# Optimization experiments

Measured on AMD Instinct MI355X. Metric: run time of the kernel, lower is better.

Reference implementation:

```python
import jax, jax.numpy as jnp
import numpy as np

NUM_BUCKETS = 32
MAX_DISTANCE = 128


def _relative_position_bucket(relative_position):
    # bidirectional=True variant of T5's bucketing
    n = -relative_position
    num_buckets = NUM_BUCKETS // 2
    ret = (n < 0).astype(jnp.int32) * num_buckets
    n = jnp.abs(n)
    max_exact = num_buckets // 2
    is_small = n < max_exact
    # log-spaced buckets for large distances
    val_if_large = max_exact + (
        jnp.log(jnp.maximum(n, 1).astype(jnp.float32) / max_exact)
        / np.log(MAX_DISTANCE / max_exact)
        * (num_buckets - max_exact)
    ).astype(jnp.int32)
    val_if_large = jnp.minimum(val_if_large, num_buckets - 1)
    return ret + jnp.where(is_small, n, val_if_large)


def setup_inputs() -> dict:
    key = jax.random.key(0)
    ks = jax.random.split(key, 6)
    B, S, D, H, DK = 4, 1024, 1024, 16, 64
    inner = H * DK
    s = 1.0 / np.sqrt(D).astype(np.float32)
    x = jax.random.normal(ks[0], (B, S, D), jnp.float32)
    Wq = jax.random.normal(ks[1], (D, inner), jnp.float32) * s
    Wk = jax.random.normal(ks[2], (D, inner), jnp.float32) * s
    Wv = jax.random.normal(ks[3], (D, inner), jnp.float32) * s
    Wo = jax.random.normal(ks[4], (inner, D), jnp.float32) * s
    rel_emb = jax.random.normal(ks[5], (NUM_BUCKETS, H), jnp.float32) * 0.02
    return {"x": x, "Wq": Wq, "Wk": Wk, "Wv": Wv, "Wo": Wo, "rel_emb": rel_emb}


def reference(x, Wq, Wk, Wv, Wo, rel_emb):
    B, S, D = x.shape
    H = rel_emb.shape[1]
    DK = Wq.shape[1] // H

    def shape_heads(t):  # [B,S,H*DK] -> [B,H,S,DK]
        return t.reshape(B, S, H, DK).transpose(0, 2, 1, 3)

    q = shape_heads(x @ Wq)
    k = shape_heads(x @ Wk)
    v = shape_heads(x @ Wv)

    # note: T5 does NOT scale by 1/sqrt(d_kv)
    scores = jnp.einsum("bhqd,bhkd->bhqk", q, k)

    pos = jnp.arange(S)
    rel = pos[None, :] - pos[:, None]            # memory - query
    bucket = _relative_position_bucket(rel)      # [S,S] int32
    bias = rel_emb[bucket].transpose(2, 0, 1)[None]  # [1,H,S,S]

    weights = jax.nn.softmax(scores + bias, axis=-1)
    ctx = jnp.einsum("bhqk,bhkd->bhqd", weights, v)
    ctx = ctx.transpose(0, 2, 1, 3).reshape(B, S, H * DK)
    return ctx @ Wo
```

## Files before the change

### kernel.cpp

```cpp
#include <hip/hip_runtime.h>
#include <math.h>

#define B_ 4
#define S_ 1024
#define D_ 1024
#define H_ 16
#define DK_ 64

typedef short bf16x8 __attribute__((ext_vector_type(8)));
typedef float f32x4 __attribute__((ext_vector_type(4)));

__device__ __forceinline__ unsigned short f2bf(float f) {
    unsigned int u = __float_as_uint(f);
    u = (u + 0x7FFFu + ((u >> 16) & 1u)) >> 16;
    return (unsigned short)u;
}

__device__ __forceinline__ float exp2_fast(float x) {
#if __has_builtin(__builtin_amdgcn_exp2f)
    return __builtin_amdgcn_exp2f(x);
#else
    return exp2f(x);
#endif
}

__device__ __forceinline__ unsigned pack_bf16(float a, float b) {
#if __has_builtin(__builtin_amdgcn_cvt_pk_bf16_f32)
    auto v = __builtin_amdgcn_cvt_pk_bf16_f32(a, b);
    return __builtin_bit_cast(unsigned int, v);
#else
    return (unsigned)f2bf(a) | ((unsigned)f2bf(b) << 16);
#endif
}

__device__ __forceinline__ float dpp_xor1(float x) {
#if __has_builtin(__builtin_amdgcn_update_dpp)
    int i = __builtin_bit_cast(int, x);
    int r = __builtin_amdgcn_update_dpp(0, i, 0xB1, 0xF, 0xF, true);
    return __builtin_bit_cast(float, r);
#else
    return __shfl_xor(x, 1);
#endif
}

__device__ __forceinline__ void gl2lds16(const void* g, void* l) {
    typedef unsigned int u32;
    auto gp = (const __attribute__((address_space(1))) u32*)(unsigned long long)g;
    auto lp = (__attribute__((address_space(3))) u32*)(unsigned int)(unsigned long long)l;
    __builtin_amdgcn_global_load_lds(gp, lp, 16, 0, 0);
}

#define LOG2E 1.44269504f
#define BIAS_OFF 20.0f

__global__ __launch_bounds__(256) void conv_all(
    const float* __restrict__ x,
    const float* __restrict__ W0, const float* __restrict__ W1,
    const float* __restrict__ W2, const float* __restrict__ W3,
    unsigned short* __restrict__ xb, unsigned short* __restrict__ Wts)
{
    __shared__ float T[32][33];
    const int t = threadIdx.x;
    const int bid = blockIdx.x;

    if (bid < 4096) {
        int i = (bid * 256 + t) * 4;
        float4 v = *(const float4*)&x[i];
        ushort4 o;
        o.x = f2bf(v.x); o.y = f2bf(v.y); o.z = f2bf(v.z); o.w = f2bf(v.w);
        *(ushort4*)&xb[i] = o;
        return;
    }
    int tile = bid - 4096;
    const int mat = tile >> 10;
    tile &= 1023;
    const float* W = (mat == 0) ? W0 : (mat == 1) ? W1 : (mat == 2) ? W2 : W3;
    unsigned short* Wt = Wts + (size_t)mat * 1048576;
    const int k0 = (tile >> 5) * 32, n0 = (tile & 31) * 32;
    {
        int r = t >> 3, c4 = (t & 7) * 4;
        float4 v = *(const float4*)&W[(size_t)(k0 + r) * D_ + n0 + c4];
        T[r][c4 + 0] = v.x; T[r][c4 + 1] = v.y; T[r][c4 + 2] = v.z; T[r][c4 + 3] = v.w;
    }
    __syncthreads();
    {
        int rn = t >> 3, c4 = (t & 7) * 4;
        ushort4 o;
        o.x = f2bf(T[c4 + 0][rn]); o.y = f2bf(T[c4 + 1][rn]);
        o.z = f2bf(T[c4 + 2][rn]); o.w = f2bf(T[c4 + 3][rn]);
        *(ushort4*)&Wt[(size_t)(n0 + rn) * D_ + k0 + c4] = o;
    }
}

__global__ __launch_bounds__(256) void gemm_qkv(
    const unsigned short* __restrict__ xb,
    const unsigned short* __restrict__ Wts,
    unsigned short* __restrict__ Qb, unsigned short* __restrict__ Kb,
    unsigned short* __restrict__ Vtb)
{
    const int bid = blockIdx.x;
    const int by = bid & 31;
    const int t_ = bid >> 5;
    const int z = t_ >> 3;
    const int bx = t_ & 7;
    const unsigned short* Bt = Wts + (size_t)z * 1048576;

    __shared__ __align__(16) unsigned short Ast[128][32];
    __shared__ __align__(16) unsigned short Bst[128][32];

    const int tid = threadIdx.x;
    const int wave = tid >> 6, lane = tid & 63;
    const int quad = lane >> 4, l16 = lane & 15;
    const int wm = (wave & 1) * 64, wn = (wave >> 1) * 64;
    const int row0 = by * 128, col0 = bx * 128;
    const int lr = lane >> 2, lc = (lane & 3) * 8;

    f32x4 acc[4][4];
#pragma unroll
    for (int i = 0; i < 4; i++)
#pragma unroll
        for (int j = 0; j < 4; j++) acc[i][j] = 0;

    for (int k0 = 0; k0 < D_; k0 += 32) {
        __syncthreads();
#pragma unroll
        for (int c = 0; c < 2; c++) {
            int m = wave * 32 + c * 16;
            gl2lds16(&xb[(size_t)(row0 + m + lr) * D_ + k0 + lc], &Ast[m][0]);
            gl2lds16(&Bt[(size_t)(col0 + m + lr) * D_ + k0 + lc], &Bst[m][0]);
        }
        __syncthreads();

        bf16x8 af[4], bfr[4];
#pragma unroll
        for (int mt = 0; mt < 4; mt++)
            af[mt] = *(const bf16x8*)&Ast[wm + mt * 16 + l16][quad * 8];
#pragma unroll
        for (int nt = 0; nt < 4; nt++)
            bfr[nt] = *(const bf16x8*)&Bst[wn + nt * 16 + l16][quad * 8];
#pragma unroll
        for (int mt = 0; mt < 4; mt++)
#pragma unroll
            for (int nt = 0; nt < 4; nt++)
                acc[mt][nt] = __builtin_amdgcn_mfma_f32_16x16x32_bf16(
                    af[mt], bfr[nt], acc[mt][nt], 0, 0, 0);
    }

    const float scale = (z == 0) ? LOG2E : 1.0f;
#pragma unroll
    for (int mt = 0; mt < 4; mt++)
#pragma unroll
        for (int nt = 0; nt < 4; nt++)
#pragma unroll
            for (int reg = 0; reg < 4; reg++) {
                int row = row0 + wm + mt * 16 + quad * 4 + reg;
                int col = col0 + wn + nt * 16 + l16;
                int b = row >> 10, s = row & 1023;
                int h = col >> 6, dk = col & 63;
                unsigned short v = f2bf(acc[mt][nt][reg] * scale);
                if (z == 0)      Qb[(((size_t)(b * H_ + h)) * S_ + s) * DK_ + dk] = v;
                else if (z == 1) Kb[(((size_t)(b * H_ + h)) * S_ + s) * DK_ + dk] = v;
                else             Vtb[(((size_t)(b * H_ + h)) * DK_ + dk) * S_ + s] = v;
            }
}

__global__ __launch_bounds__(256) void gemm_out(
    const unsigned short* __restrict__ Ab,
    const unsigned short* __restrict__ Bt,
    float* __restrict__ out)
{
    const int bid = blockIdx.x;
    const int by = bid & 63;
    const int bx = bid >> 6;

    __shared__ __align__(16) unsigned short Ast[64][32];
    __shared__ __align__(16) unsigned short Bst[128][32];

    const int tid = threadIdx.x;
    const int wave = tid >> 6, lane = tid & 63;
    const int quad = lane >> 4, l16 = lane & 15;
    const int wm = (wave & 1) * 32, wn = (wave >> 1) * 64;
    const int row0 = by * 64, col0 = bx * 128;
    const int lr = lane >> 2, lc = (lane & 3) * 8;

    f32x4 acc[2][4];
#pragma unroll
    for (int i = 0; i < 2; i++)
#pragma unroll
        for (int j = 0; j < 4; j++) acc[i][j] = 0;

    for (int k0 = 0; k0 < D_; k0 += 32) {
        __syncthreads();
        gl2lds16(&Ab[(size_t)(row0 + wave * 16 + lr) * D_ + k0 + lc],
                 &Ast[wave * 16][0]);
#pragma unroll
        for (int c = 0; c < 2; c++) {
            int m = (wave * 2 + c) * 16;
            gl2lds16(&Bt[(size_t)(col0 + m + lr) * D_ + k0 + lc], &Bst[m][0]);
        }
        __syncthreads();

        bf16x8 af[2], bfr[4];
#pragma unroll
        for (int mt = 0; mt < 2; mt++)
            af[mt] = *(const bf16x8*)&Ast[wm + mt * 16 + l16][quad * 8];
#pragma unroll
        for (int nt = 0; nt < 4; nt++)
            bfr[nt] = *(const bf16x8*)&Bst[wn + nt * 16 + l16][quad * 8];
#pragma unroll
        for (int mt = 0; mt < 2; mt++)
#pragma unroll
            for (int nt = 0; nt < 4; nt++)
                acc[mt][nt] = __builtin_amdgcn_mfma_f32_16x16x32_bf16(
                    af[mt], bfr[nt], acc[mt][nt], 0, 0, 0);
    }

#pragma unroll
    for (int mt = 0; mt < 2; mt++)
#pragma unroll
        for (int nt = 0; nt < 4; nt++)
#pragma unroll
            for (int reg = 0; reg < 4; reg++) {
                int row = row0 + wm + mt * 16 + quad * 4 + reg;
                int col = col0 + wn + nt * 16 + l16;
                out[(size_t)row * D_ + col] = acc[mt][nt][reg];
            }
}

__global__ __launch_bounds__(256) void attn_mfma(
    const unsigned short* __restrict__ Qb, const unsigned short* __restrict__ Kb,
    const unsigned short* __restrict__ Vtb, const float* __restrict__ rel_emb,
    unsigned short* __restrict__ CTXb)
{
    __shared__ __align__(16) unsigned short Ks[2][128][64];
    __shared__ __align__(16) unsigned short Vts[2][64][128];
    __shared__ __align__(16) unsigned short Pw[4][16][40];
    __shared__ float bias_tab[2047];

    const int bid = blockIdx.x;
    const int bh = bid & 63;
    const int b = bh >> 4, h = bh & 15;
    const int q0 = (bid >> 6) * 128;
    const int tid = threadIdx.x;
    const int wave = tid >> 6, lane = tid & 63;
    const int quad = lane >> 4, l16 = lane & 15;
    const int qw = q0 + wave * 32;

    for (int idx = tid; idx < 2047; idx += 256) {
        int rel = idx - 1023;
        int n = -rel, ret = 0;
        if (n < 0) { ret = 16; n = -n; }
        int bkt;
        if (n < 8) bkt = ret + n;
        else {
            float t = logf((float)n / 8.0f) / logf(16.0f) * 8.0f;
            int v = 8 + (int)t;
            if (v > 15) v = 15;
            bkt = ret + v;
        }
        bias_tab[idx] = rel_emb[bkt * H_ + h] * LOG2E - BIAS_OFF;
    }

    const size_t hb = (size_t)(b * H_ + h) * (S_ * DK_);
    const unsigned short* Qp = Qb + hb;
    const unsigned short* Kp = Kb + hb;
    const unsigned short* Vp = Vtb + hb;

    bf16x8 qf[2][2];
#pragma unroll
    for (int sub = 0; sub < 2; sub++)
#pragma unroll
        for (int ks = 0; ks < 2; ks++)
            qf[sub][ks] = *(const bf16x8*)
                &Qp[(size_t)(qw + sub * 16 + l16) * DK_ + ks * 32 + quad * 8];

    f32x4 O[2][4];
#pragma unroll
    for (int sub = 0; sub < 2; sub++)
#pragma unroll
        for (int dt = 0; dt < 4; dt++) O[sub][dt] = 0;
    float lsum[2][4] = {{0.f, 0.f, 0.f, 0.f}, {0.f, 0.f, 0.f, 0.f}};

    const int pcol = (l16 & 1) ? (8 + (l16 >> 1)) : (l16 >> 1);
    unsigned* pwp = (unsigned*)&Pw[wave][0][0];
    const int swz = l16 & 7;

    const int kr8 = lane >> 3;
    const int kck = ((lane & 7) ^ kr8) * 8;
    const int vr4 = lane >> 4;
    auto stageKV = [&](int db, int k0) {
#pragma unroll
        for (int i = 0; i < 4; i++) {
            int blk = wave * 4 + i;
            gl2lds16(&Kp[(size_t)(k0 + blk * 8 + kr8) * DK_ + kck],
                     &Ks[db][blk * 8][0]);
            int vrow = blk * 4 + vr4;
            int vck = ((lane & 15) ^ (vrow & 7)) * 8;
            gl2lds16(&Vp[(size_t)vrow * S_ + k0 + vck],
                     &Vts[db][blk * 4][0]);
        }
    };

    stageKV(0, 0);

    for (int kt = 0; kt < 8; kt++) {
        const int k0 = kt * 128;
        const int db = kt & 1;
        __syncthreads();
        if (kt < 7) stageKV(db ^ 1, k0 + 128);

#pragma unroll
        for (int nt2 = 0; nt2 < 4; nt2++) {
            bf16x8 kf[2][2], vf[4];
#pragma unroll
            for (int t = 0; t < 2; t++) {
                int row = (2 * nt2 + t) * 16 + l16;
#pragma unroll
                for (int ks = 0; ks < 2; ks++)
                    kf[t][ks] = *(const bf16x8*)
                        &Ks[db][row][((ks * 4 + quad) ^ swz) * 8];
            }
#pragma unroll
            for (int dt = 0; dt < 4; dt++)
                vf[dt] = *(const bf16x8*)
                    &Vts[db][dt * 16 + l16][((nt2 * 4 + quad) ^ swz) * 8];

#pragma unroll
            for (int sub = 0; sub < 2; sub++) {
                const int sb = qw + sub * 16;
                f32x4 sacc[2];
#pragma unroll
                for (int t = 0; t < 2; t++) {
                    int b0 = 1023 + k0 + (2 * nt2 + t) * 16 + l16 - (sb + quad * 4 + 3);
                    float bl[4];
#pragma unroll
                    for (int j = 0; j < 4; j++) bl[j] = bias_tab[b0 + j];
#pragma unroll
                    for (int reg = 0; reg < 4; reg++) sacc[t][reg] = bl[3 - reg];
                }
                __builtin_amdgcn_s_setprio(1);
#pragma unroll
                for (int ks = 0; ks < 2; ks++)
#pragma unroll
                    for (int t = 0; t < 2; t++)
                        sacc[t] = __builtin_amdgcn_mfma_f32_16x16x32_bf16(
                            qf[sub][ks], kf[t][ks], sacc[t], 0, 0, 0);
                __builtin_amdgcn_s_setprio(0);

#pragma unroll
                for (int reg = 0; reg < 4; reg++) {
                    float pa = exp2_fast(sacc[0][reg]);
                    float pb = exp2_fast(sacc[1][reg]);
                    lsum[sub][reg] += pa + pb;
                    float pax = dpp_xor1(pa), pbx = dpp_xor1(pb);
                    unsigned ue = pack_bf16(pa, pax);
                    unsigned uo = pack_bf16(pbx, pb);
                    pwp[(quad * 4 + reg) * 20 + pcol] = (l16 & 1) ? uo : ue;
                }

                bf16x8 pf = *(const bf16x8*)&Pw[wave][l16][quad * 8];
                __builtin_amdgcn_s_setprio(1);
#pragma unroll
                for (int dt = 0; dt < 4; dt++)
                    O[sub][dt] = __builtin_amdgcn_mfma_f32_16x16x32_bf16(
                        pf, vf[dt], O[sub][dt], 0, 0, 0);
                __builtin_amdgcn_s_setprio(0);
            }
        }
    }

#pragma unroll
    for (int sub = 0; sub < 2; sub++)
#pragma unroll
        for (int reg = 0; reg < 4; reg++) {
            float l = lsum[sub][reg];
#pragma unroll
            for (int off = 1; off < 16; off <<= 1)
                l += __shfl_xor(l, off);
            float inv = 1.0f / l;
            int s = qw + sub * 16 + quad * 4 + reg;
#pragma unroll
            for (int dt = 0; dt < 4; dt++) {
                int col = h * DK_ + dt * 16 + l16;
                CTXb[((size_t)(b * S_ + s)) * D_ + col] = f2bf(O[sub][dt][reg] * inv);
            }
        }
}

extern "C" void kernel_launch(void* const* d_in, const int* in_sizes, int n_in,
                              void* d_out, int out_size, void* d_ws, size_t ws_size,
                              hipStream_t stream) {
    const float* x   = (const float*)d_in[0];
    const float* Wq  = (const float*)d_in[1];
    const float* Wk  = (const float*)d_in[2];
    const float* Wv  = (const float*)d_in[3];
    const float* Wo  = (const float*)d_in[4];
    const float* rel = (const float*)d_in[5];
    float* out = (float*)d_out;

    unsigned short* ws = (unsigned short*)d_ws;
    unsigned short* xb   = ws;
    unsigned short* Wts  = ws + (size_t)4194304;
    unsigned short* Qb   = ws + (size_t)8388608;
    unsigned short* Kb   = ws + (size_t)12582912;
    unsigned short* Vtb  = ws + (size_t)16777216;
    unsigned short* CTXb = ws + (size_t)20971520;

    conv_all<<<8192, 256, 0, stream>>>(x, Wq, Wk, Wv, Wo, xb, Wts);
    gemm_qkv<<<768, 256, 0, stream>>>(xb, Wts, Qb, Kb, Vtb);
    attn_mfma<<<512, 256, 0, stream>>>(Qb, Kb, Vtb, rel, CTXb);
    gemm_out<<<512, 256, 0, stream>>>(CTXb, Wts + (size_t)3 * 1048576, out);
}
```

Before: 186.7 us.

## Compute transposed scores and build P fragment in registers via permlane swaps

Swaps MFMA operands so the score tile comes out transposed, which lets each lane hold exp values for a fixed query row. The P operand for the PV MFMA is then assembled with cvt_pk_bf16 and permlane32/16 swaps instead of a round trip through the per-wave LDS buffer, and the row sum becomes a per-lane scalar reduced at the end. This is meant to remove LDS write/read traffic and waits in the inner loop, at the cost of relying on gfx950-specific permlane swap instructions and inline asm.

```diff
diff --git a/kernel.cpp b/kernel.cpp
--- a/kernel.cpp
+++ b/kernel.cpp
@@ -24,23 +24,10 @@
 #endif
 }
 
-__device__ __forceinline__ unsigned pack_bf16(float a, float b) {
-#if __has_builtin(__builtin_amdgcn_cvt_pk_bf16_f32)
-    auto v = __builtin_amdgcn_cvt_pk_bf16_f32(a, b);
-    return __builtin_bit_cast(unsigned int, v);
-#else
-    return (unsigned)f2bf(a) | ((unsigned)f2bf(b) << 16);
-#endif
-}
-
-__device__ __forceinline__ float dpp_xor1(float x) {
-#if __has_builtin(__builtin_amdgcn_update_dpp)
-    int i = __builtin_bit_cast(int, x);
-    int r = __builtin_amdgcn_update_dpp(0, i, 0xB1, 0xF, 0xF, true);
-    return __builtin_bit_cast(float, r);
-#else
-    return __shfl_xor(x, 1);
-#endif
+__device__ __forceinline__ int cvt_pk_bf16(float lo, float hi) {
+    int r;
+    asm("v_cvt_pk_bf16_f32 %0, %1, %2" : "=v"(r) : "v"(lo), "v"(hi));
+    return r;
 }
 
 __device__ __forceinline__ void gl2lds16(const void* g, void* l) {
@@ -234,7 +221,6 @@
 {
     __shared__ __align__(16) unsigned short Ks[2][128][64];
     __shared__ __align__(16) unsigned short Vts[2][64][128];
-    __shared__ __align__(16) unsigned short Pw[4][16][40];
     __shared__ float bias_tab[2047];
 
     const int bid = blockIdx.x;
@@ -279,10 +265,8 @@
     for (int sub = 0; sub < 2; sub++)
 #pragma unroll
         for (int dt = 0; dt < 4; dt++) O[sub][dt] = 0;
-    float lsum[2][4] = {{0.f, 0.f, 0.f, 0.f}, {0.f, 0.f, 0.f, 0.f}};
-
-    const int pcol = (l16 & 1) ? (8 + (l16 >> 1)) : (l16 >> 1);
-    unsigned* pwp = (unsigned*)&Pw[wave][0][0];
+    float lsum[2] = {0.f, 0.f};
+
     const int swz = l16 & 7;
 
     const int kr8 = lane >> 3;
@@ -327,16 +311,14 @@
 
 #pragma unroll
             for (int sub = 0; sub < 2; sub++) {
-                const int sb = qw + sub * 16;
                 f32x4 sacc[2];
 #pragma unroll
                 for (int t = 0; t < 2; t++) {
-                    int b0 = 1023 + k0 + (2 * nt2 + t) * 16 + l16 - (sb + quad * 4 + 3);
-                    float bl[4];
-#pragma unroll
-                    for (int j = 0; j < 4; j++) bl[j] = bias_tab[b0 + j];
-#pragma unroll
-                    for (int reg = 0; reg < 4; reg++) sacc[t][reg] = bl[3 - reg];
+                    int b0 = 1023 + k0 + (2 * nt2 + t) * 16 + quad * 4
+                             - (qw + sub * 16 + l16);
+#pragma unroll
+                    for (int reg = 0; reg < 4; reg++)
+                        sacc[t][reg] = bias_tab[b0 + reg];
                 }
                 __builtin_amdgcn_s_setprio(1);
 #pragma unroll
@@ -344,21 +326,29 @@
 #pragma unroll
                     for (int t = 0; t < 2; t++)
                         sacc[t] = __builtin_amdgcn_mfma_f32_16x16x32_bf16(
-                            qf[sub][ks], kf[t][ks], sacc[t], 0, 0, 0);
+                            kf[t][ks], qf[sub][ks], sacc[t], 0, 0, 0);
                 __builtin_amdgcn_s_setprio(0);
 
+                float e0[4], e1[4];
 #pragma unroll
                 for (int reg = 0; reg < 4; reg++) {
-                    float pa = exp2_fast(sacc[0][reg]);
-                    float pb = exp2_fast(sacc[1][reg]);
-                    lsum[sub][reg] += pa + pb;
-                    float pax = dpp_xor1(pa), pbx = dpp_xor1(pb);
-                    unsigned ue = pack_bf16(pa, pax);
-                    unsigned uo = pack_bf16(pbx, pb);
-                    pwp[(quad * 4 + reg) * 20 + pcol] = (l16 & 1) ? uo : ue;
+                    e0[reg] = exp2_fast(sacc[0][reg]);
+                    e1[reg] = exp2_fast(sacc[1][reg]);
                 }
-
-                bf16x8 pf = *(const bf16x8*)&Pw[wave][l16][quad * 8];
+                lsum[sub] += (e0[0] + e0[1]) + (e0[2] + e0[3])
+                           + (e1[0] + e1[1]) + (e1[2] + e1[3]);
+
+                int x0 = cvt_pk_bf16(e0[0], e0[1]);
+                int x1 = cvt_pk_bf16(e0[2], e0[3]);
+                int x2 = cvt_pk_bf16(e1[0], e1[1]);
+                int x3 = cvt_pk_bf16(e1[2], e1[3]);
+                asm("v_permlane32_swap_b32 %0, %1" : "+v"(x0), "+v"(x2));
+                asm("v_permlane32_swap_b32 %0, %1" : "+v"(x1), "+v"(x3));
+                asm("v_permlane16_swap_b32 %0, %1" : "+v"(x0), "+v"(x2));
+                asm("v_permlane16_swap_b32 %0, %1" : "+v"(x1), "+v"(x3));
+                int4 pi; pi.x = x0; pi.y = x1; pi.z = x2; pi.w = x3;
+                bf16x8 pf = __builtin_bit_cast(bf16x8, pi);
+
                 __builtin_amdgcn_s_setprio(1);
 #pragma unroll
                 for (int dt = 0; dt < 4; dt++)
@@ -370,14 +360,14 @@
     }
 
 #pragma unroll
-    for (int sub = 0; sub < 2; sub++)
+    for (int sub = 0; sub < 2; sub++) {
+        float l = lsum[sub];
+        l += __shfl_xor(l, 16);
+        l += __shfl_xor(l, 32);
+        float invl = 1.0f / l;
 #pragma unroll
         for (int reg = 0; reg < 4; reg++) {
-            float l = lsum[sub][reg];
-#pragma unroll
-            for (int off = 1; off < 16; off <<= 1)
-                l += __shfl_xor(l, off);
-            float inv = 1.0f / l;
+            float inv = __shfl(invl, quad * 4 + reg);
             int s = qw + sub * 16 + quad * 4 + reg;
 #pragma unroll
             for (int dt = 0; dt < 4; dt++) {
@@ -385,6 +375,7 @@
                 CTXb[((size_t)(b * S_ + s)) * D_ + col] = f2bf(O[sub][dt][reg] * inv);
             }
         }
+    }
 }
 
 extern "C" void kernel_launch(void* const* d_in, const int* in_sizes, int n_in,
```

Measured after the change: 177.0 us. 1.05x faster.
